# Optimization experiments

Measured on AMD Instinct MI355X. Metric: run time of the kernel, lower is better.

The kernel has to match this reference:

```python
import jax, jax.numpy as jnp
import numpy as np
from jax import lax

T_DATA = 20000
E_NO = 2000
I_NO = 500
SUB_NO = 16
SYN_B = 3
HID = 256
T_SYN = 200
T_ENC = 80


def _causal_conv(x, kern):
    # x: [T, S] per-subunit drive; kern: [S, K] causal kernels (index = lag)
    S, K = kern.shape
    lhs = jnp.pad(x.T, ((0, 0), (K - 1, 0)))[None]        # [1, S, T+K-1]
    rhs = kern[:, ::-1][:, None, :]                        # flip then correlate == torch conv1d path
    out = lax.conv_general_dilated(lhs, rhs, (1,), 'VALID', feature_group_count=S)
    return out[0].T                                        # [T, S]


def setup_inputs() -> dict:
    key = jax.random.key(0)
    ks = jax.random.split(key, 16)
    V_in = jax.random.normal(ks[0], (T_DATA,), jnp.float32) * 5.0 - 69.0
    S_e = jax.random.bernoulli(ks[1], 0.02, (T_DATA, E_NO)).astype(jnp.float32)
    S_i = jax.random.bernoulli(ks[2], 0.02, (T_DATA, I_NO)).astype(jnp.float32)
    # synapse -> subunit one-hot assignment matrices [sub_no, n_syn]
    C_syn_e = jax.nn.one_hot(jax.random.randint(ks[3], (E_NO,), 0, SUB_NO), SUB_NO, dtype=jnp.float32).T
    C_syn_i = jax.nn.one_hot(jax.random.randint(ks[4], (I_NO,), 0, SUB_NO), SUB_NO, dtype=jnp.float32).T
    # parameters, initialized exactly as in __init__
    K_syn = jnp.stack([jnp.full((SUB_NO, SYN_B), 0.04),
                       jnp.full((SUB_NO, SYN_B), -0.02),
                       jnp.full((SUB_NO, SYN_B), 0.02)], axis=-1)          # [sub, B, 3]
    tau_syn = jnp.tile((jnp.arange(SYN_B, dtype=jnp.float32) + 1.6)[:, None], (1, 3))  # [B, 3]
    delta_syn = jnp.full((SUB_NO, 2), 2.0, jnp.float32)
    enc_bias = jnp.zeros((SUB_NO - 1,), jnp.float32)
    W_in = 2 * T_ENC - 1

    def lin(k, fan_out, fan_in):
        kw, kb = jax.random.split(k)
        s = 1.0 / np.sqrt(fan_in)
        return (jax.random.uniform(kw, (fan_out, fan_in), jnp.float32, -s, s),
                jax.random.uniform(kb, (fan_out,), jnp.float32, -s, s))

    W1, b1 = lin(ks[5], HID, W_in)
    W2, b2 = lin(ks[6], HID, HID)
    W3, b3 = lin(ks[7], HID, HID)
    W4, b4 = lin(ks[8], SUB_NO - 1, HID)
    a1 = jnp.float32(0.25)
    a2 = jnp.float32(0.25)
    a3 = jnp.float32(0.25)
    return dict(V_in=V_in, S_e=S_e, S_i=S_i, C_syn_e=C_syn_e, C_syn_i=C_syn_i,
                K_syn=K_syn, tau_syn=tau_syn, delta_syn=delta_syn, enc_bias=enc_bias,
                W1=W1, b1=b1, a1=a1, W2=W2, b2=b2, a2=a2, W3=W3, b3=b3, a3=a3,
                W4=W4, b4=b4)


def reference(V_in, S_e, S_i, C_syn_e, C_syn_i, K_syn, tau_syn, delta_syn, enc_bias,
              W1, b1, a1, W2, b2, a2, W3, b3, a3, W4, b4):
    T = V_in.shape[0]
    # ---- spike_convolve, fully vectorized over (subunit, basis) ----
    t = jnp.arange(T_SYN, dtype=V_in.dtype)                 # [T_syn]
    d = jnp.exp(delta_syn)                                   # [sub, 2]
    te = jnp.maximum(t[None, :] - d[:, 0:1], 0.0)            # [sub, T_syn]
    ti = jnp.maximum(t[None, :] - d[:, 1:2], 0.0)
    tau = jnp.exp(tau_syn)                                   # [B, 3]
    tte = te[:, None, :] / tau[None, :, 0, None]             # [sub, B, T_syn]
    tti = ti[:, None, :] / tau[None, :, 1, None]
    ker_e = jnp.einsum('sbt,sb->st', tte * jnp.exp(-tte), K_syn[:, :, 0])
    ker_i = jnp.einsum('sbt,sb->st', tti * jnp.exp(-tti), K_syn[:, :, 1])
    in_e = S_e @ C_syn_e.T                                   # [T, sub]
    in_i = S_i @ C_syn_i.T
    S_conv = _causal_conv(in_e, ker_e) + _causal_conv(in_i, ker_i)   # [T, sub]
    # ---- encode: batched sliding-window MLP (replaces per-timestep loop) ----
    W = 2 * T_ENC - 1
    Vpad = jnp.zeros((T + W,), V_in.dtype).at[T_ENC - 1:T_ENC - 1 + T].set(V_in)
    idx = jnp.arange(T)[:, None] + jnp.arange(W)[None, :]    # [T, W]
    win = Vpad[idx]                                          # [T, W]
    prelu = lambda x, a: jnp.where(x >= 0, x, a * x)
    h = prelu(win @ W1.T + b1, a1)
    h = prelu(h @ W2.T + b2, a2)
    h = prelu(h @ W3.T + b3, a3)
    nn_out = h @ W4.T + b4                                   # [T, sub-1]
    return jax.nn.sigmoid(nn_out + S_conv[:, 1:] + enc_bias)
```

## Files before the change

### kernel.cpp

```cpp
#include <hip/hip_runtime.h>
#include <cstdint>
#include <cstddef>

#define T_DATA 20000
#define E_NO 2000
#define I_NO 500
#define SUB_NO 16
#define HID 256
#define T_SYN 200
#define T_ENC 80
#define W_IN 159

typedef __attribute__((ext_vector_type(8))) __bf16 bf16x8;
typedef __attribute__((ext_vector_type(8))) short short8;
typedef __attribute__((ext_vector_type(4))) float floatx4;
typedef __attribute__((ext_vector_type(4))) unsigned int uint4v;
typedef __attribute__((ext_vector_type(2))) unsigned int uint2v;

__device__ __forceinline__ float bf2f(unsigned short u) {
    union { unsigned int i; float f; } v; v.i = ((unsigned int)u) << 16; return v.f;
}
__device__ __forceinline__ unsigned short f2bf(float f) {
    union { float f; unsigned int i; } v; v.f = f;
    unsigned int r = v.i + 0x7FFFu + ((v.i >> 16) & 1u);
    return (unsigned short)(r >> 16);
}
__device__ __forceinline__ float inload(const void* p, int i, int isbf) {
    return isbf ? bf2f(((const unsigned short*)p)[i]) : ((const float*)p)[i];
}

__device__ __forceinline__ int detect_bf(const void* Se, int* sfl) {
    if (threadIdx.x == 0) *sfl = 0;
    __syncthreads();
    const unsigned int* w = (const unsigned int*)Se;
    int la = 0;
    #pragma unroll
    for (int i = 0; i < 4; i++)
        la |= (w[i * 256 + threadIdx.x] & 0xFFFFu) ? 1 : 0;
    if (la) atomicOr(sfl, 1);
    __syncthreads();
    return *sfl;
}

#define OFF_KERE   16u
#define OFF_KERI   12816u
#define OFF_W1H    25616u
#define OFF_W1L    107536u
#define OFF_W2H    189456u
#define OFF_W2L    320528u
#define OFF_W3H    451600u
#define OFF_W3L    582672u
#define OFF_W4H    713744u
#define OFF_W4L    721424u
#define OFF_INE    729104u
#define OFF_INI    1049104u

#define SPIKE_BLOCKS 1250
#define SETUP_BLOCKS 712

__device__ __forceinline__ bf16x8 hi_pack(uint4v u0, uint4v u1) {
    uint4v r;
    r[0] = (u0[0] >> 16) | (u0[1] & 0xFFFF0000u);
    r[1] = (u0[2] >> 16) | (u0[3] & 0xFFFF0000u);
    r[2] = (u1[0] >> 16) | (u1[1] & 0xFFFF0000u);
    r[3] = (u1[2] >> 16) | (u1[3] & 0xFFFF0000u);
    return __builtin_bit_cast(bf16x8, r);
}
template<bool BF>
__device__ __forceinline__ bf16x8 ldfrag(const void* p, size_t idx) {
    if (BF) return *(const bf16x8*)((const unsigned short*)p + idx);
    const float* f = (const float*)p + idx;
    return hi_pack(*(const uint4v*)f, *(const uint4v*)(f + 4));
}
template<bool BF>
__device__ __forceinline__ bf16x8 ldfrag4(const void* p, size_t idx) {
    uint4v r = {0u, 0u, 0u, 0u};
    if (BF) {
        uint2v u = *(const uint2v*)((const unsigned short*)p + idx);
        r[0] = u[0]; r[1] = u[1];
    } else {
        uint4v u = *(const uint4v*)((const float*)p + idx);
        r[0] = (u[0] >> 16) | (u[1] & 0xFFFF0000u);
        r[1] = (u[2] >> 16) | (u[3] & 0xFFFF0000u);
    }
    return __builtin_bit_cast(bf16x8, r);
}

template<bool BF>
__device__ __forceinline__ void spike_gemm(const void* Se, const void* Si,
        const void* Ce, const void* Ci,
        unsigned char* in_e, unsigned char* in_i, float* red) {
    int tid = threadIdx.x;
    int lane = tid & 63, wave = tid >> 6;
    int lm = lane & 15, quad = lane >> 4;
    int t0 = blockIdx.x * 16;
    size_t teb = (size_t)(t0 + lm) * E_NO;
    size_t tib = (size_t)(t0 + lm) * I_NO;
    floatx4 ae = {0.f, 0.f, 0.f, 0.f}, ai = {0.f, 0.f, 0.f, 0.f};
    short8 zs = {0, 0, 0, 0, 0, 0, 0, 0};
    bf16x8 bz = __builtin_bit_cast(bf16x8, zs);

    #pragma unroll
    for (int q = 0; q < 16; q++) {
        int kg = wave * 16 + q;
        int k0 = kg * 32 + quad * 8;
        bf16x8 a = bz, b = bz;
        if (kg < 63 && (kg < 62 || quad < 2)) {
            a = ldfrag<BF>(Ce, (size_t)lm * E_NO + k0);
            b = ldfrag<BF>(Se, teb + k0);
        }
        ae = __builtin_amdgcn_mfma_f32_16x16x32_bf16(a, b, ae, 0, 0, 0);
    }
    #pragma unroll
    for (int q = 0; q < 4; q++) {
        int kg = wave * 4 + q;
        int k0 = kg * 32 + quad * 8;
        bf16x8 a = bz, b = bz;
        if (kg < 15 || quad < 2) {
            a = ldfrag<BF>(Ci, (size_t)lm * I_NO + k0);
            b = ldfrag<BF>(Si, tib + k0);
        } else if (quad == 2) {
            a = ldfrag4<BF>(Ci, (size_t)lm * I_NO + k0);
            b = ldfrag4<BF>(Si, tib + k0);
        }
        ai = __builtin_amdgcn_mfma_f32_16x16x32_bf16(a, b, ai, 0, 0, 0);
    }
    float* re = red;
    float* ri = red + 1024;
    #pragma unroll
    for (int j = 0; j < 4; j++) {
        re[wave * 256 + (quad * 4 + j) * 16 + lm] = ae[j];
        ri[wave * 256 + (quad * 4 + j) * 16 + lm] = ai[j];
    }
    __syncthreads();
    if (tid < 64) {
        int t = tid >> 2, qd = tid & 3;
        unsigned pe = 0, pi = 0;
        #pragma unroll
        for (int j = 0; j < 4; j++) {
            float se_ = 0.f, si_ = 0.f;
            #pragma unroll
            for (int w = 0; w < 4; w++) {
                se_ += re[w * 256 + (qd * 4 + j) * 16 + t];
                si_ += ri[w * 256 + (qd * 4 + j) * 16 + t];
            }
            pe |= ((unsigned)(se_ + 0.5f) & 0xFFu) << (8 * j);
            pi |= ((unsigned)(si_ + 0.5f) & 0xFFu) << (8 * j);
        }
        ((unsigned*)in_e)[(t0 + t) * 4 + qd] = pe;
        ((unsigned*)in_i)[(t0 + t) * 4 + qd] = pi;
    }
}

__global__ void __launch_bounds__(256) k_front(
        const void* Se, const void* Si, const void* Ce, const void* Ci,
        const void* Ksyn, const void* tau_syn, const void* dly,
        const void* W1, const void* W2, const void* W3, const void* W4,
        float* ker_e, float* ker_i,
        unsigned short* W1h, unsigned short* W1l,
        unsigned short* W2h, unsigned short* W2l,
        unsigned short* W3h, unsigned short* W3l,
        unsigned short* W4h, unsigned short* W4l,
        unsigned char* in_e, unsigned char* in_i) {
    __shared__ int sfl;
    __shared__ __align__(16) float red[2048];
    int f = detect_bf(Se, &sfl);
    int tid = threadIdx.x;

    if (blockIdx.x < SPIKE_BLOCKS) {
        if (f) spike_gemm<true>(Se, Si, Ce, Ci, in_e, in_i, red);
        else   spike_gemm<false>(Se, Si, Ce, Ci, in_e, in_i, red);
    } else {
        int id = (blockIdx.x - SPIKE_BLOCKS) * 256 + tid;
        if (id < 6400) {
            int c = id < 3200 ? 0 : 1;
            int q = id - c * 3200;
            int s = q / 200, j = q - s * 200;
            float d = expf(inload(dly, s * 2 + c, f));
            float tt = fmaxf((float)j - d, 0.0f);
            float acc = 0.f;
            #pragma unroll
            for (int b = 0; b < 3; b++) {
                float tau = expf(inload(tau_syn, b * 3 + c, f));
                float x = tt / tau;
                acc += x * expf(-x) * inload(Ksyn, (s * 3 + b) * 3 + c, f);
            }
            (c == 0 ? ker_e : ker_i)[s * 200 + j] = acc;
        } else if (id < 47360) {
            int q = id - 6400;
            int n = q / 160, k = q - n * 160;
            float v = (k < W_IN) ? inload(W1, n * W_IN + k, f) : 0.f;
            unsigned short hi = f2bf(v);
            W1h[q] = hi;
            W1l[q] = f2bf(v - bf2f(hi));
        } else if (id < 112896) {
            int q = id - 47360;
            float v = inload(W2, q, f);
            unsigned short hi = f2bf(v);
            W2h[q] = hi;
            W2l[q] = f2bf(v - bf2f(hi));
        } else if (id < 178432) {
            int q = id - 112896;
            float v = inload(W3, q, f);
            unsigned short hi = f2bf(v);
            W3h[q] = hi;
            W3l[q] = f2bf(v - bf2f(hi));
        } else if (id < 182272) {
            int q = id - 178432;
            float v = inload(W4, q, f);
            unsigned short hi = f2bf(v);
            W4h[q] = hi;
            W4l[q] = f2bf(v - bf2f(hi));
        }
    }
}

template<bool BF>
__device__ __forceinline__ void mlp_body(
    const void* V,
    const unsigned short* W1h, const unsigned short* W1l, const void* b1, const void* a1p,
    const unsigned short* W2h, const unsigned short* W2l, const void* b2, const void* a2p,
    const unsigned short* W3h, const unsigned short* W3l, const void* b3, const void* a3p,
    const unsigned short* W4h, const unsigned short* W4l, const void* b4,
    const void* encb, const float* sc, void* out,
    unsigned short* Ahi, unsigned short* Alo)
{
    int tid = threadIdx.x;
    int lane = tid & 63, wave = tid >> 6;
    int lm = lane & 15, quad = lane >> 4;
    int t0 = blockIdx.x * 64;

    auto ld = [&](const void* p, int i) -> float {
        return BF ? bf2f(((const unsigned short*)p)[i]) : ((const float*)p)[i];
    };

    for (int idx = tid; idx < 64 * 160; idx += 256) {
        int m = idx / 160, k = idx - m * 160;
        int tg = t0 + m + k - (T_ENC - 1);
        float v = 0.f;
        if (k < W_IN && tg >= 0 && tg < T_DATA) v = ld(V, tg);
        unsigned short hi = f2bf(v);
        int col = (((k >> 3) ^ (m & 31)) << 3) | (k & 7);
        Ahi[m * 256 + col] = hi;
        if (!BF) Alo[m * 256 + col] = f2bf(v - bf2f(hi));
    }
    __syncthreads();

    floatx4 acc[4][4];
    auto aoff = [&](int mt, int ks) {
        int arow = mt * 16 + lm;
        return arow * 256 + ((((ks << 2) | quad) ^ (arow & 31)) << 3);
    };

    auto epi = [&](const void* bias, float alpha) {
        __syncthreads();
        #pragma unroll
        for (int mt = 0; mt < 4; mt++) {
            #pragma unroll
            for (int nt = 0; nt < 4; nt++) {
                int cn = wave * 64 + nt * 16 + lm;
                float bb = ld(bias, cn);
                #pragma unroll
                for (int j = 0; j < 4; j++) {
                    int row = mt * 16 + quad * 4 + j;
                    float h = acc[mt][nt][j] + bb;
                    h = (h >= 0.f) ? h : alpha * h;
                    unsigned short hi = f2bf(h);
                    int col = (((cn >> 3) ^ (row & 31)) << 3) | (cn & 7);
                    Ahi[row * 256 + col] = hi;
                    if (!BF) Alo[row * 256 + col] = f2bf(h - bf2f(hi));
                }
            }
        }
        __syncthreads();
    };

    floatx4 z = {0.f, 0.f, 0.f, 0.f};
    {
        #pragma unroll
        for (int mt = 0; mt < 4; mt++)
            #pragma unroll
            for (int nt = 0; nt < 4; nt++) acc[mt][nt] = z;
        if (BF) {
            bf16x8 Bh[5][4];
            #pragma unroll
            for (int ks = 0; ks < 5; ks++)
                #pragma unroll
                for (int nt = 0; nt < 4; nt++)
                    Bh[ks][nt] = *(const bf16x8*)(W1h + (size_t)(wave * 64 + nt * 16 + lm) * 160 + ks * 32 + quad * 8);
            #pragma unroll
            for (int ks = 0; ks < 5; ks++) {
                bf16x8 a[4];
                #pragma unroll
                for (int mt = 0; mt < 4; mt++) a[mt] = *(const bf16x8*)&Ahi[aoff(mt, ks)];
                #pragma unroll
                for (int nt = 0; nt < 4; nt++)
                    #pragma unroll
                    for (int mt = 0; mt < 4; mt++)
                        acc[mt][nt] = __builtin_amdgcn_mfma_f32_16x16x32_bf16(a[mt], Bh[ks][nt], acc[mt][nt], 0, 0, 0);
            }
        } else {
            for (int ks = 0; ks < 5; ks++) {
                bf16x8 ah[4], al[4];
                #pragma unroll
                for (int mt = 0; mt < 4; mt++) {
                    ah[mt] = *(const bf16x8*)&Ahi[aoff(mt, ks)];
                    al[mt] = *(const bf16x8*)&Alo[aoff(mt, ks)];
                }
                #pragma unroll
                for (int nt = 0; nt < 4; nt++) {
                    size_t bo = (size_t)(wave * 64 + nt * 16 + lm) * 160 + ks * 32 + quad * 8;
                    bf16x8 bh = *(const bf16x8*)(W1h + bo);
                    bf16x8 bl = *(const bf16x8*)(W1l + bo);
                    #pragma unroll
                    for (int mt = 0; mt < 4; mt++) {
                        acc[mt][nt] = __builtin_amdgcn_mfma_f32_16x16x32_bf16(ah[mt], bh, acc[mt][nt], 0, 0, 0);
                        acc[mt][nt] = __builtin_amdgcn_mfma_f32_16x16x32_bf16(al[mt], bh, acc[mt][nt], 0, 0, 0);
                        acc[mt][nt] = __builtin_amdgcn_mfma_f32_16x16x32_bf16(ah[mt], bl, acc[mt][nt], 0, 0, 0);
                    }
                }
            }
        }
        epi(b1, ld(a1p, 0));
    }
    const unsigned short* Whs[2] = {W2h, W3h};
    const unsigned short* Wls[2] = {W2l, W3l};
    const void* bs[2] = {b2, b3};
    const void* as_[2] = {a2p, a3p};
    for (int l = 0; l < 2; l++) {
        #pragma unroll
        for (int mt = 0; mt < 4; mt++)
            #pragma unroll
            for (int nt = 0; nt < 4; nt++) acc[mt][nt] = z;
        const unsigned short* Wh = Whs[l];
        const unsigned short* Wl = Wls[l];
        if (BF) {
            bf16x8 Bh[8][4];
            #pragma unroll
            for (int ks = 0; ks < 8; ks++)
                #pragma unroll
                for (int nt = 0; nt < 4; nt++)
                    Bh[ks][nt] = *(const bf16x8*)(Wh + (size_t)(wave * 64 + nt * 16 + lm) * 256 + ks * 32 + quad * 8);
            #pragma unroll
            for (int ks = 0; ks < 8; ks++) {
                bf16x8 a[4];
                #pragma unroll
                for (int mt = 0; mt < 4; mt++) a[mt] = *(const bf16x8*)&Ahi[aoff(mt, ks)];
                #pragma unroll
                for (int nt = 0; nt < 4; nt++)
                    #pragma unroll
                    for (int mt = 0; mt < 4; mt++)
                        acc[mt][nt] = __builtin_amdgcn_mfma_f32_16x16x32_bf16(a[mt], Bh[ks][nt], acc[mt][nt], 0, 0, 0);
            }
        } else {
            for (int ks = 0; ks < 8; ks++) {
                bf16x8 ah[4], al[4];
                #pragma unroll
                for (int mt = 0; mt < 4; mt++) {
                    ah[mt] = *(const bf16x8*)&Ahi[aoff(mt, ks)];
                    al[mt] = *(const bf16x8*)&Alo[aoff(mt, ks)];
                }
                #pragma unroll
                for (int nt = 0; nt < 4; nt++) {
                    size_t bo = (size_t)(wave * 64 + nt * 16 + lm) * 256 + ks * 32 + quad * 8;
                    bf16x8 bh = *(const bf16x8*)(Wh + bo);
                    bf16x8 bl = *(const bf16x8*)(Wl + bo);
                    #pragma unroll
                    for (int mt = 0; mt < 4; mt++) {
                        acc[mt][nt] = __builtin_amdgcn_mfma_f32_16x16x32_bf16(ah[mt], bh, acc[mt][nt], 0, 0, 0);
                        acc[mt][nt] = __builtin_amdgcn_mfma_f32_16x16x32_bf16(al[mt], bh, acc[mt][nt], 0, 0, 0);
                        acc[mt][nt] = __builtin_amdgcn_mfma_f32_16x16x32_bf16(ah[mt], bl, acc[mt][nt], 0, 0, 0);
                    }
                }
            }
        }
        epi(bs[l], ld(as_[l], 0));
    }
    {
        int mt = wave;
        short8 z8 = {0, 0, 0, 0, 0, 0, 0, 0};
        bf16x8 bz = __builtin_bit_cast(bf16x8, z8);
        floatx4 a4 = z;
        #pragma unroll
        for (int ks = 0; ks < 8; ks++) {
            bf16x8 ah = *(const bf16x8*)&Ahi[aoff(mt, ks)];
            bf16x8 bh = bz;
            if (lm < 15)
                bh = *(const bf16x8*)(W4h + (size_t)lm * 256 + ks * 32 + quad * 8);
            a4 = __builtin_amdgcn_mfma_f32_16x16x32_bf16(ah, bh, a4, 0, 0, 0);
            if (!BF) {
                bf16x8 al = *(const bf16x8*)&Alo[aoff(mt, ks)];
                bf16x8 bl = bz;
                if (lm < 15)
                    bl = *(const bf16x8*)(W4l + (size_t)lm * 256 + ks * 32 + quad * 8);
                a4 = __builtin_amdgcn_mfma_f32_16x16x32_bf16(al, bh, a4, 0, 0, 0);
                a4 = __builtin_amdgcn_mfma_f32_16x16x32_bf16(ah, bl, a4, 0, 0, 0);
            }
        }
        if (lm < 15) {
            float bb = ld(b4, lm) + ld(encb, lm);
            #pragma unroll
            for (int j = 0; j < 4; j++) {
                int row = mt * 16 + quad * 4 + j;
                int t = t0 + row;
                if (t < T_DATA) {
                    float x = a4[j] + bb + sc[row * 16 + lm + 1];
                    x = fminf(fmaxf(x, -40.f), 40.f);
                    float sg = 1.f / (1.f + expf(-x));
                    if (BF) ((unsigned short*)out)[(size_t)t * 15 + lm] = f2bf(sg);
                    else    ((float*)out)[(size_t)t * 15 + lm] = sg;
                }
            }
        }
    }
}

__global__ void __launch_bounds__(256, 2) k_back(
    const void* Se, const void* V,
    const unsigned char* in_e, const unsigned char* in_i,
    const float* ker_e, const float* ker_i,
    const unsigned short* W1h, const unsigned short* W1l, const void* b1, const void* a1p,
    const unsigned short* W2h, const unsigned short* W2l, const void* b2, const void* a2p,
    const unsigned short* W3h, const unsigned short* W3l, const void* b3, const void* a3p,
    const unsigned short* W4h, const unsigned short* W4l, const void* b4,
    const void* encb, void* out) {
    __shared__ __align__(16) char smem[65536];
    __shared__ __align__(16) float sc[64 * 16];
    __shared__ int sfl;
    int f = detect_bf(Se, &sfl);
    int tid = threadIdx.x;
    int t0 = blockIdx.x * 64;

    {
        float* se = (float*)smem;
        float* si = se + 263 * 17;
        float* ke = si + 263 * 17;
        float* ki = ke + 16 * 201;
        for (int idx = tid; idx < 263 * 4; idx += 256) {
            int r = idx >> 2, wi = idx & 3;
            int t = t0 - 199 + r;
            unsigned int ve = 0, vi = 0;
            if (t >= 0 && t < T_DATA) {
                ve = ((const unsigned int*)in_e)[t * 4 + wi];
                vi = ((const unsigned int*)in_i)[t * 4 + wi];
            }
            #pragma unroll
            for (int b = 0; b < 4; b++) {
                se[r * 17 + wi * 4 + b] = (float)((ve >> (8 * b)) & 0xFF);
                si[r * 17 + wi * 4 + b] = (float)((vi >> (8 * b)) & 0xFF);
            }
        }
        for (int idx = tid; idx < 3200; idx += 256) {
            int s = idx / 200, j = idx - s * 200;
            ke[s * 201 + j] = ker_e[idx];
            ki[s * 201 + j] = ker_i[idx];
        }
        __syncthreads();
        int s = tid & 15, g4 = (tid >> 4) * 4;
        float a0 = 0.f, a1 = 0.f, a2 = 0.f, a3 = 0.f;
        float w0 = se[(g4 + 199) * 17 + s], w1 = se[(g4 + 200) * 17 + s];
        float w2 = se[(g4 + 201) * 17 + s], w3 = se[(g4 + 202) * 17 + s];
        float x0 = si[(g4 + 199) * 17 + s], x1 = si[(g4 + 200) * 17 + s];
        float x2 = si[(g4 + 201) * 17 + s], x3 = si[(g4 + 202) * 17 + s];
        #pragma unroll 4
        for (int j = 0; j < 200; j++) {
            float kej = ke[s * 201 + j];
            float kij = ki[s * 201 + j];
            a0 += w0 * kej + x0 * kij;
            a1 += w1 * kej + x1 * kij;
            a2 += w2 * kej + x2 * kij;
            a3 += w3 * kej + x3 * kij;
            int lr = g4 + 198 - j; lr = lr < 0 ? 0 : lr;
            float nw = se[lr * 17 + s], nx = si[lr * 17 + s];
            w3 = w2; w2 = w1; w1 = w0; w0 = nw;
            x3 = x2; x2 = x1; x1 = x0; x0 = nx;
        }
        sc[(g4 + 0) * 16 + s] = a0;
        sc[(g4 + 1) * 16 + s] = a1;
        sc[(g4 + 2) * 16 + s] = a2;
        sc[(g4 + 3) * 16 + s] = a3;
        __syncthreads();
    }

    unsigned short* Ahi = (unsigned short*)smem;
    unsigned short* Alo = Ahi + 64 * 256;
    if (f)
        mlp_body<true>(V, W1h, W1l, b1, a1p, W2h, W2l, b2, a2p, W3h, W3l, b3, a3p,
                       W4h, W4l, b4, encb, sc, out, Ahi, Alo);
    else
        mlp_body<false>(V, W1h, W1l, b1, a1p, W2h, W2l, b2, a2p, W3h, W3l, b3, a3p,
                        W4h, W4l, b4, encb, sc, out, Ahi, Alo);
}

extern "C" void kernel_launch(void* const* d_in, const int* in_sizes, int n_in,
                              void* d_out, int out_size, void* d_ws, size_t ws_size,
                              hipStream_t stream) {
    const void* V    = d_in[0];
    const void* Se   = d_in[1];
    const void* Si   = d_in[2];
    const void* Ce   = d_in[3];
    const void* Ci   = d_in[4];
    const void* Ksyn = d_in[5];
    const void* tau  = d_in[6];
    const void* dly  = d_in[7];
    const void* encb = d_in[8];
    const void* W1   = d_in[9];
    const void* b1   = d_in[10];
    const void* a1   = d_in[11];
    const void* W2   = d_in[12];
    const void* b2   = d_in[13];
    const void* a2   = d_in[14];
    const void* W3   = d_in[15];
    const void* b3   = d_in[16];
    const void* a3   = d_in[17];
    const void* W4   = d_in[18];
    const void* b4   = d_in[19];

    char* w = (char*)d_ws;
    float* ker_e = (float*)(w + OFF_KERE);
    float* ker_i = (float*)(w + OFF_KERI);
    unsigned short* W1h = (unsigned short*)(w + OFF_W1H);
    unsigned short* W1l = (unsigned short*)(w + OFF_W1L);
    unsigned short* W2h = (unsigned short*)(w + OFF_W2H);
    unsigned short* W2l = (unsigned short*)(w + OFF_W2L);
    unsigned short* W3h = (unsigned short*)(w + OFF_W3H);
    unsigned short* W3l = (unsigned short*)(w + OFF_W3L);
    unsigned short* W4h = (unsigned short*)(w + OFF_W4H);
    unsigned short* W4l = (unsigned short*)(w + OFF_W4L);
    unsigned char* in_e = (unsigned char*)(w + OFF_INE);
    unsigned char* in_i = (unsigned char*)(w + OFF_INI);

    k_front<<<SPIKE_BLOCKS + SETUP_BLOCKS, 256, 0, stream>>>(
        Se, Si, Ce, Ci, Ksyn, tau, dly, W1, W2, W3, W4,
        ker_e, ker_i, W1h, W1l, W2h, W2l, W3h, W3l, W4h, W4l, in_e, in_i);
    k_back<<<313, 256, 0, stream>>>(
        Se, V, in_e, in_i, ker_e, ker_i,
        W1h, W1l, b1, a1, W2h, W2l, b2, a2, W3h, W3l, b3, a3,
        W4h, W4l, b4, encb, d_out);
}
```

Baseline: 377.9 us.

## Give each wave its own time tile in spike GEMM and drop cross-wave reduction

The spike-count GEMM used to split the K dimension across four waves per 16-row time tile, then reduce the partial sums through shared memory behind a block barrier. Now each wave owns a full 16-row time tile and loops over the whole K range, so the block covers 64 rows and needs four times fewer spike blocks. This removes the cross-wave reduction and its __syncthreads. The bf16 path adds a three-deep register prefetch of MFMA operands to hide load latency. In exchange each wave runs a much longer serial MFMA chain and the grid has fewer blocks, which may leave loads less parallel. A wave writes its shared scratch and reads it back from other lanes with no barrier, relying on wave-level ordering.

```diff
diff --git a/kernel.cpp b/kernel.cpp
--- a/kernel.cpp
+++ b/kernel.cpp
@@ -55,7 +55,7 @@
 #define OFF_INE    729104u
 #define OFF_INI    1049104u
 
-#define SPIKE_BLOCKS 1250
+#define SPIKE_BLOCKS 313
 #define SETUP_BLOCKS 712
 
 __device__ __forceinline__ bf16x8 hi_pack(uint4v u0, uint4v u1) {
@@ -89,66 +89,83 @@
 template<bool BF>
 __device__ __forceinline__ void spike_gemm(const void* Se, const void* Si,
         const void* Ce, const void* Ci,
-        unsigned char* in_e, unsigned char* in_i, float* red) {
+        unsigned char* in_e, unsigned char* in_i, unsigned char* scr) {
     int tid = threadIdx.x;
     int lane = tid & 63, wave = tid >> 6;
     int lm = lane & 15, quad = lane >> 4;
-    int t0 = blockIdx.x * 16;
-    size_t teb = (size_t)(t0 + lm) * E_NO;
-    size_t tib = (size_t)(t0 + lm) * I_NO;
+    int tw = blockIdx.x * 64 + wave * 16;
+    int trow = tw + lm; if (trow > T_DATA - 1) trow = T_DATA - 1;
+    size_t teb = (size_t)trow * E_NO;
+    size_t tib = (size_t)trow * I_NO;
+    size_t ceb = (size_t)lm * E_NO;
+    size_t cib = (size_t)lm * I_NO;
     floatx4 ae = {0.f, 0.f, 0.f, 0.f}, ai = {0.f, 0.f, 0.f, 0.f};
     short8 zs = {0, 0, 0, 0, 0, 0, 0, 0};
     bf16x8 bz = __builtin_bit_cast(bf16x8, zs);
 
-    #pragma unroll
-    for (int q = 0; q < 16; q++) {
-        int kg = wave * 16 + q;
-        int k0 = kg * 32 + quad * 8;
-        bf16x8 a = bz, b = bz;
-        if (kg < 63 && (kg < 62 || quad < 2)) {
-            a = ldfrag<BF>(Ce, (size_t)lm * E_NO + k0);
-            b = ldfrag<BF>(Se, teb + k0);
-        }
-        ae = __builtin_amdgcn_mfma_f32_16x16x32_bf16(a, b, ae, 0, 0, 0);
-    }
-    #pragma unroll
-    for (int q = 0; q < 4; q++) {
-        int kg = wave * 4 + q;
-        int k0 = kg * 32 + quad * 8;
-        bf16x8 a = bz, b = bz;
-        if (kg < 15 || quad < 2) {
-            a = ldfrag<BF>(Ci, (size_t)lm * I_NO + k0);
-            b = ldfrag<BF>(Si, tib + k0);
-        } else if (quad == 2) {
-            a = ldfrag4<BF>(Ci, (size_t)lm * I_NO + k0);
-            b = ldfrag4<BF>(Si, tib + k0);
-        }
-        ai = __builtin_amdgcn_mfma_f32_16x16x32_bf16(a, b, ai, 0, 0, 0);
-    }
-    float* re = red;
-    float* ri = red + 1024;
+    auto ldAE = [&](int kg) -> bf16x8 {
+        if (kg == 62 && quad >= 2) return bz;
+        return ldfrag<BF>(Ce, ceb + kg * 32 + quad * 8);
+    };
+    auto ldBE = [&](int kg) -> bf16x8 {
+        if (kg == 62 && quad >= 2) return bz;
+        return ldfrag<BF>(Se, teb + kg * 32 + quad * 8);
+    };
+    if (BF) {
+        bf16x8 aR[3], bR[3];
+        #pragma unroll
+        for (int q = 0; q < 3; q++) { aR[q] = ldAE(q); bR[q] = ldBE(q); }
+        #pragma unroll
+        for (int kg = 0; kg < 63; kg++) {
+            int s = kg % 3;
+            ae = __builtin_amdgcn_mfma_f32_16x16x32_bf16(aR[s], bR[s], ae, 0, 0, 0);
+            int nk = kg + 3;
+            if (nk < 63) { aR[s] = ldAE(nk); bR[s] = ldBE(nk); }
+        }
+    } else {
+        #pragma unroll 2
+        for (int kg = 0; kg < 63; kg++) {
+            bf16x8 a = ldAE(kg), b = ldBE(kg);
+            ae = __builtin_amdgcn_mfma_f32_16x16x32_bf16(a, b, ae, 0, 0, 0);
+        }
+    }
+    auto ldAI = [&](int kg) -> bf16x8 {
+        if (kg < 15 || quad < 2) return ldfrag<BF>(Ci, cib + kg * 32 + quad * 8);
+        if (quad == 2) return ldfrag4<BF>(Ci, cib + kg * 32 + quad * 8);
+        return bz;
+    };
+    auto ldBI = [&](int kg) -> bf16x8 {
+        if (kg < 15 || quad < 2) return ldfrag<BF>(Si, tib + kg * 32 + quad * 8);
+        if (quad == 2) return ldfrag4<BF>(Si, tib + kg * 32 + quad * 8);
+        return bz;
+    };
+    if (BF) {
+        bf16x8 aR[3], bR[3];
+        #pragma unroll
+        for (int q = 0; q < 3; q++) { aR[q] = ldAI(q); bR[q] = ldBI(q); }
+        #pragma unroll
+        for (int kg = 0; kg < 16; kg++) {
+            int s = kg % 3;
+            ai = __builtin_amdgcn_mfma_f32_16x16x32_bf16(aR[s], bR[s], ai, 0, 0, 0);
+            int nk = kg + 3;
+            if (nk < 16) { aR[s] = ldAI(nk); bR[s] = ldBI(nk); }
+        }
+    } else {
+        #pragma unroll 2
+        for (int kg = 0; kg < 16; kg++) {
+            bf16x8 a = ldAI(kg), b = ldBI(kg);
+            ai = __builtin_amdgcn_mfma_f32_16x16x32_bf16(a, b, ai, 0, 0, 0);
+        }
+    }
+    unsigned char* sw = scr + wave * 1024;
     #pragma unroll
     for (int j = 0; j < 4; j++) {
-        re[wave * 256 + (quad * 4 + j) * 16 + lm] = ae[j];
-        ri[wave * 256 + (quad * 4 + j) * 16 + lm] = ai[j];
-    }
-    __syncthreads();
-    if (tid < 64) {
-        int t = tid >> 2, qd = tid & 3;
-        unsigned pe = 0, pi = 0;
-        #pragma unroll
-        for (int j = 0; j < 4; j++) {
-            float se_ = 0.f, si_ = 0.f;
-            #pragma unroll
-            for (int w = 0; w < 4; w++) {
-                se_ += re[w * 256 + (qd * 4 + j) * 16 + t];
-                si_ += ri[w * 256 + (qd * 4 + j) * 16 + t];
-            }
-            pe |= ((unsigned)(se_ + 0.5f) & 0xFFu) << (8 * j);
-            pi |= ((unsigned)(si_ + 0.5f) & 0xFFu) << (8 * j);
-        }
-        ((unsigned*)in_e)[(t0 + t) * 4 + qd] = pe;
-        ((unsigned*)in_i)[(t0 + t) * 4 + qd] = pi;
+        sw[lm * 16 + quad * 4 + j]       = (unsigned char)(int)(ae[j] + 0.5f);
+        sw[256 + lm * 16 + quad * 4 + j] = (unsigned char)(int)(ai[j] + 0.5f);
+    }
+    if (tw + (lane >> 2) < T_DATA) {
+        ((unsigned*)in_e)[(size_t)tw * 4 + lane] = *(const unsigned*)&sw[lane * 4];
+        ((unsigned*)in_i)[(size_t)tw * 4 + lane] = *(const unsigned*)&sw[256 + lane * 4];
     }
 }
 
@@ -163,13 +180,13 @@
         unsigned short* W4h, unsigned short* W4l,
         unsigned char* in_e, unsigned char* in_i) {
     __shared__ int sfl;
-    __shared__ __align__(16) float red[2048];
+    __shared__ __align__(16) unsigned char scr[4096];
     int f = detect_bf(Se, &sfl);
     int tid = threadIdx.x;
 
     if (blockIdx.x < SPIKE_BLOCKS) {
-        if (f) spike_gemm<true>(Se, Si, Ce, Ci, in_e, in_i, red);
-        else   spike_gemm<false>(Se, Si, Ce, Ci, in_e, in_i, red);
+        if (f) spike_gemm<true>(Se, Si, Ce, Ci, in_e, in_i, scr);
+        else   spike_gemm<false>(Se, Si, Ce, Ci, in_e, in_i, scr);
     } else {
         int id = (blockIdx.x - SPIKE_BLOCKS) * 256 + tid;
         if (id < 6400) {
```

After: 401.6 us. 6.3% more time.
